# Optimization experiments

Measured on AMD Instinct MI355X. Metric: run time of the kernel, lower is better.

Reference implementation:

```python
import jax, jax.numpy as jnp
import numpy as np

EMBED_DIM = 1024
HEADS = 16
HEAD_DIM = EMBED_DIM // HEADS
N, SEQ = 2, 2048


def setup_inputs() -> dict:
    key = jax.random.key(0)
    ks = jax.random.split(key, 9)
    s = 1.0 / np.sqrt(HEAD_DIM)
    inp = {
        "values": jax.random.normal(ks[0], (N, SEQ, EMBED_DIM), jnp.float32),
        "keys": jax.random.normal(ks[1], (N, SEQ, EMBED_DIM), jnp.float32),
        "query": jax.random.normal(ks[2], (N, SEQ, EMBED_DIM), jnp.float32),
        "mask": jax.random.randint(ks[3], (N, 1, SEQ, SEQ), 0, 2, jnp.int32),
        # per-head projection weights (torch Linear: y = x @ W.T)
        "Wv": jax.random.normal(ks[4], (HEAD_DIM, HEAD_DIM), jnp.float32) * s,
        "Wk": jax.random.normal(ks[5], (HEAD_DIM, HEAD_DIM), jnp.float32) * s,
        "Wq": jax.random.normal(ks[6], (HEAD_DIM, HEAD_DIM), jnp.float32) * s,
        "Wo": jax.random.normal(ks[7], (EMBED_DIM, EMBED_DIM), jnp.float32) * (1.0 / np.sqrt(EMBED_DIM)),
        "bo": jax.random.normal(ks[8], (EMBED_DIM,), jnp.float32) * 0.01,
    }
    return inp


def reference(values, keys, query, mask, Wv, Wk, Wq, Wo, bo):
    n, q_len = query.shape[0], query.shape[1]
    v_len, k_len = values.shape[1], keys.shape[1]
    # reshape to [N, len, H, D]
    v = values.reshape(n, v_len, HEADS, HEAD_DIM)
    k = keys.reshape(n, k_len, HEADS, HEAD_DIM)
    q = query.reshape(n, q_len, HEADS, HEAD_DIM)
    # per-head linear projections (shared weight across heads), torch: x @ W.T
    v = jnp.einsum("nlhd,ed->nlhe", v, Wv)
    k = jnp.einsum("nlhd,ed->nlhe", k, Wk)
    q = jnp.einsum("nlhd,ed->nlhe", q, Wq)
    # energy: [N, H, Q, K]
    energy = jnp.einsum("nqhd,nkhd->nhqk", q, k)
    energy = jnp.where(mask == 0, jnp.float32(-1e20), energy)
    # NOTE: original scales by sqrt(embed_dim), not sqrt(head_dim)
    attention = jax.nn.softmax(energy / jnp.sqrt(jnp.float32(EMBED_DIM)), axis=3)
    out = jnp.einsum("nhql,nlhd->nqhd", attention, v).reshape(n, q_len, EMBED_DIM)
    out = out @ Wo.T + bo  # fc_out; dropout is identity in eval mode
    return out
```

## Files before the change

### kernel.cpp

```cpp
#include <hip/hip_runtime.h>
#include <hip/hip_bf16.h>

#define NB 2
#define SEQ 2048
#define HEADS 16
#define HD 64
#define ED 1024

typedef __bf16 bf16x8 __attribute__((ext_vector_type(8)));
typedef float f32x4 __attribute__((ext_vector_type(4)));
typedef unsigned short u16x8 __attribute__((ext_vector_type(8)));
typedef unsigned short u16x4 __attribute__((ext_vector_type(4)));

#if __has_builtin(__builtin_amdgcn_exp2f)
#define EXP2(x) __builtin_amdgcn_exp2f(x)
#else
#define EXP2(x) __builtin_exp2f(x)
#endif

__device__ __forceinline__ unsigned short f2bf(float f) {
    unsigned u = __builtin_bit_cast(unsigned, f);
    u += 0x7fffu + ((u >> 16) & 1u);
    return (unsigned short)(u >> 16);
}

__device__ __forceinline__ bf16x8 cvt8(const float* __restrict__ p) {
    const float4* p4 = (const float4*)p;
    float4 a = p4[0], b = p4[1];
    u16x8 u;
    u[0] = f2bf(a.x); u[1] = f2bf(a.y); u[2] = f2bf(a.z); u[3] = f2bf(a.w);
    u[4] = f2bf(b.x); u[5] = f2bf(b.y); u[6] = f2bf(b.z); u[7] = f2bf(b.w);
    return __builtin_bit_cast(bf16x8, u);
}

__device__ __forceinline__ bf16x8 ldfrag(const void* p) {
    uint4 v = *(const uint4*)p;
    return __builtin_bit_cast(bf16x8, v);
}

__device__ __forceinline__ f32x4 mfma16(bf16x8 a, bf16x8 b, f32x4 c) {
    return __builtin_amdgcn_mfma_f32_16x16x32_bf16(a, b, c, 0, 0, 0);
}

__device__ __forceinline__ unsigned packbf(float lo, float hi) {
    unsigned a = __builtin_bit_cast(unsigned, hi) + 0x8000u;
    unsigned b = __builtin_bit_cast(unsigned, lo) + 0x8000u;
    return __builtin_amdgcn_perm(a, b, 0x07060302u);
}

#define GLOAD_LDS(gp, lp) \
    __builtin_amdgcn_global_load_lds( \
        (const __attribute__((address_space(1))) unsigned int*)(gp), \
        (__attribute__((address_space(3))) unsigned int*)(lp), 16, 0, 0)

#define QSCALE 0.04508422f

__global__ __launch_bounds__(256) void proj_prep_kernel(
    const float* __restrict__ qin, const float* __restrict__ kin, const float* __restrict__ vin,
    const float* __restrict__ Wq, const float* __restrict__ Wk, const float* __restrict__ Wv,
    unsigned short* __restrict__ Qb, unsigned short* __restrict__ Kb,
    unsigned short* __restrict__ Vt,
    const int* __restrict__ mask, unsigned long long* __restrict__ bits,
    const float* __restrict__ Wo, unsigned short* __restrict__ Wob)
{
    __shared__ __align__(16) char tile[64 * 144];

    int bid = blockIdx.x;
    if (bid >= 3072) {
        int b2 = bid - 3072;
        if (b2 < NB * SEQ * SEQ / 256) {
            size_t i = (size_t)b2 * 256 + threadIdx.x;
            int m = mask[i];
            unsigned long long b = __ballot(m != 0);
            if ((threadIdx.x & 63) == 0) bits[i >> 6] = b;
        } else {
            size_t i = ((size_t)(b2 - NB * SEQ * SEQ / 256) * 256 + threadIdx.x) * 4;
            float4 v = *(const float4*)(Wo + i);
            u16x4 u;
            u[0] = f2bf(v.x); u[1] = f2bf(v.y); u[2] = f2bf(v.z); u[3] = f2bf(v.w);
            *(u16x4*)(Wob + i) = u;
        }
        return;
    }

    int t3  = bid >> 10;
    int rem = bid & 1023;
    int h   = rem >> 6;
    int rt  = rem & 63;
    int wave = threadIdx.x >> 6, lane = threadIdx.x & 63;
    int quad = lane >> 4, l16 = lane & 15;

    const float* in = (t3 == 0) ? qin : ((t3 == 1) ? kin : vin);
    const float* W  = (t3 == 0) ? Wq  : ((t3 == 1) ? Wk  : Wv);

    int r0 = rt * 64 + wave * 16;

    bf16x8 bf0[4], bf1[4];
#pragma unroll
    for (int sl = 0; sl < 4; ++sl) {
        const float* wrow = W + (sl * 16 + l16) * 64;
        bf0[sl] = cvt8(wrow + quad * 8);
        bf1[sl] = cvt8(wrow + 32 + quad * 8);
    }
    const float* xrow = in + (size_t)(r0 + l16) * ED + h * 64;
    bf16x8 af0 = cvt8(xrow + quad * 8);
    bf16x8 af1 = cvt8(xrow + 32 + quad * 8);

    f32x4 acc[4];
#pragma unroll
    for (int sl = 0; sl < 4; ++sl) {
        f32x4 c = {0.f, 0.f, 0.f, 0.f};
        c = mfma16(af0, bf0[sl], c);
        c = mfma16(af1, bf1[sl], c);
        acc[sl] = c;
    }
    float sc = (t3 == 0) ? QSCALE : 1.0f;

    size_t nh = (size_t)((r0 >> 11) * HEADS + h);
    int rl = lane >> 3, cl = lane & 7;

    if (t3 != 2) {
#pragma unroll
        for (int r = 0; r < 4; ++r) {
            int srow = wave * 16 + quad * 4 + r;
#pragma unroll
            for (int sl = 0; sl < 4; ++sl)
                *(unsigned short*)(tile + srow * 144 + (sl * 16 + l16) * 2) =
                    f2bf(acc[sl][r] * sc);
        }
        unsigned short* dst = (t3 == 0) ? Qb : Kb;
        int s0 = (r0 & 2047);
#pragma unroll
        for (int g = 0; g < 2; ++g) {
            int lrow = wave * 16 + g * 8 + rl;
            uint4 v = *(const uint4*)(tile + lrow * 144 + cl * 16);
            *(uint4*)(dst + (nh * SEQ + (s0 & ~15) + g * 8 + rl) * HD + cl * 8) = v;
        }
    } else {
#pragma unroll
        for (int r = 0; r < 4; ++r) {
            int srow = wave * 16 + quad * 4 + r;
#pragma unroll
            for (int sl = 0; sl < 4; ++sl)
                *(unsigned short*)(tile + (sl * 16 + l16) * 144 + srow * 2) =
                    f2bf(acc[sl][r]);
        }
        __syncthreads();
        int s_tile = rt & 31;
#pragma unroll
        for (int g = 0; g < 2; ++g) {
            int erow = wave * 16 + g * 8 + rl;
            uint4 v = *(const uint4*)(tile + erow * 144 + cl * 16);
            *(uint4*)(Vt + ((nh * 32 + s_tile) * 64 + erow) * 64 + cl * 8) = v;
        }
    }
}

__global__ __launch_bounds__(256, 4) void attn_kernel(
    const unsigned short* __restrict__ Qb, const unsigned short* __restrict__ Kb,
    const unsigned short* __restrict__ Vt2, const unsigned long long* __restrict__ mb,
    unsigned short* __restrict__ Ab)
{
    __shared__ __align__(16) char smem[24576 + 4 * 2304];

    int tid = threadIdx.x;
    int wave = tid >> 6, lane = tid & 63;
    int quad = lane >> 4, l16 = lane & 15;

    int b   = blockIdx.x;
    int xcd = b & 7;
    int j   = b >> 3;
    int nh  = xcd * 4 + (j >> 5);
    int qb  = j & 31;
    int n = nh >> 4, h = nh & 15;
    int q0 = qb * 64 + wave * 16;

    size_t headoff = (size_t)nh * SEQ * HD;
    const unsigned short* qrow = Qb + headoff + (size_t)(q0 + l16) * HD;
    bf16x8 qf0 = ldfrag(qrow + quad * 8);
    bf16x8 qf1 = ldfrag(qrow + 32 + quad * 8);

    int srow = lane >> 3, sslot = lane & 7;
    int stoff = srow * 128 + (((sslot - srow) & 7) * 16);

    int rotA = ((quad + l16) & 7) * 16;
    int aK0 = l16 * 128 + rotA;
    int aV  = 16384 + l16 * 128 + rotA;
    int aVx = aV ^ 64;
    char* pbase = smem + 24576 + wave * 2304;
    char* pw = pbase + l16 * 144 + quad * 8;
    char* pr = pbase + l16 * 144 + quad * 16;

    const unsigned short* gK = Kb + headoff;
    const unsigned short* gV = Vt2 + (size_t)nh * (32 * 4096);
    const unsigned long long* mbase = mb + (size_t)n * (SEQ * SEQ / 64)
                                         + (size_t)(q0 + l16) * (SEQ / 64);

    u16x8 ou;
#pragma unroll
    for (int jj = 0; jj < 8; ++jj) ou[jj] = 0x3F80;
    bf16x8 ones = __builtin_bit_cast(bf16x8, ou);

    f32x4 o[4] = {{0,0,0,0},{0,0,0,0},{0,0,0,0},{0,0,0,0}};
    f32x4 lacc = {0,0,0,0};
    int qsh = quad * 4;

    {
        const char* sK = (const char*)gK + stoff;
        const char* sV = (const char*)gV + stoff;
#pragma unroll
        for (int i2 = 0; i2 < 2; ++i2) {
            int c = wave * 2 + i2;
            GLOAD_LDS(sK + c * 1024, smem + c * 1024);
            GLOAD_LDS(sV + c * 1024, smem + 16384 + c * 1024);
        }
    }

    int par = 0;
    for (int kb = 0; kb < SEQ; kb += 64) {
        int kbn = (kb + 64) & (SEQ - 1);
        __syncthreads();
        {
            const char* sK = (const char*)(gK + (size_t)kbn * 64) + stoff;
            char* dK = smem + (par ^ 1) * 8192;
#pragma unroll
            for (int i2 = 0; i2 < 2; ++i2) {
                int c = wave * 2 + i2;
                GLOAD_LDS(sK + c * 1024, dK + c * 1024);
            }
        }
        unsigned long long m64 = mbase[kb >> 6] >> qsh;

        const char* kbuf = smem + par * 8192;
        bf16x8 kf[4][2];
#pragma unroll
        for (int kt = 0; kt < 4; ++kt) {
            kf[kt][0] = ldfrag(kbuf + aK0 + kt * 2048);
            kf[kt][1] = ldfrag(kbuf + (aK0 ^ 64) + kt * 2048);
        }
        f32x4 c[4];
#pragma unroll
        for (int kt = 0; kt < 4; ++kt) {
            f32x4 cc = {0.f, 0.f, 0.f, 0.f};
            cc = mfma16(kf[kt][0], qf0, cc);
            cc = mfma16(kf[kt][1], qf1, cc);
            c[kt] = cc;
        }
        unsigned mlo = (unsigned)m64;
        unsigned mhi = (unsigned)(m64 >> 32);
#pragma unroll
        for (int kt = 0; kt < 4; ++kt) {
            unsigned mw = (kt & 2) ? mhi : mlo;
            int bs = (kt & 1) ? 16 : 0;
            float p0 = ((mw >> (bs + 0)) & 1u) ? EXP2(c[kt][0]) : 0.f;
            float p1 = ((mw >> (bs + 1)) & 1u) ? EXP2(c[kt][1]) : 0.f;
            float p2 = ((mw >> (bs + 2)) & 1u) ? EXP2(c[kt][2]) : 0.f;
            float p3 = ((mw >> (bs + 3)) & 1u) ? EXP2(c[kt][3]) : 0.f;
            uint2 dw = { packbf(p0, p1), packbf(p2, p3) };
            *(uint2*)(pw + kt * 32) = dw;
        }
        bf16x8 pb0 = ldfrag(pr);
        bf16x8 pb1 = ldfrag(pr + 64);
        lacc = mfma16(ones, pb0, lacc);
        lacc = mfma16(ones, pb1, lacc);
#pragma unroll
        for (int sl = 0; sl < 4; ++sl) {
            o[sl] = mfma16(ldfrag(smem + aV  + sl * 2048), pb0, o[sl]);
            o[sl] = mfma16(ldfrag(smem + aVx + sl * 2048), pb1, o[sl]);
        }
        __syncthreads();
        {
            const char* sV = (const char*)(gV + (size_t)(kbn >> 6) * 4096) + stoff;
#pragma unroll
            for (int i2 = 0; i2 < 2; ++i2) {
                int c = wave * 2 + i2;
                GLOAD_LDS(sV + c * 1024, smem + 16384 + c * 1024);
            }
        }
        par ^= 1;
    }

    {
        float rinv = 1.0f / lacc[0];
        int q = q0 + l16;
        unsigned short* op = Ab + (((size_t)(n * SEQ + q)) * HEADS + h) * HD + qsh;
#pragma unroll
        for (int sl = 0; sl < 4; ++sl) {
            u16x4 u;
            u[0] = f2bf(o[sl][0] * rinv);
            u[1] = f2bf(o[sl][1] * rinv);
            u[2] = f2bf(o[sl][2] * rinv);
            u[3] = f2bf(o[sl][3] * rinv);
            *(u16x4*)(op + sl * 16) = u;
        }
    }
}

__global__ __launch_bounds__(256) void out_gemm_kernel(
    const unsigned short* __restrict__ Ab, const unsigned short* __restrict__ Wob,
    const float* __restrict__ bo, float* __restrict__ out)
{
    __shared__ __align__(16) char lds[49152];

    int tid = threadIdx.x;
    int wave = tid >> 6, lane = tid & 63;
    int quad = lane >> 4, l16 = lane & 15;
    int rt = blockIdx.x >> 4, ct = blockIdx.x & 15;
    int wr = wave >> 1, wc = wave & 1;

    int srow = lane >> 3, sslot = lane & 7;
    int stoff = srow * 2048 + (((sslot - srow) & 7) * 16);
    const char* gA = (const char*)Ab  + (size_t)rt * 128 * 2048 + stoff;
    const char* gB = (const char*)Wob + (size_t)ct * 64 * 2048 + stoff;

    int aA[4], aB[2];
#pragma unroll
    for (int i = 0; i < 4; ++i) {
        int rowA = wr * 64 + i * 16 + l16;
        aA[i] = rowA * 128 + (((quad + rowA) & 7) * 16);
    }
#pragma unroll
    for (int sl = 0; sl < 2; ++sl) {
        int rowB = wc * 32 + sl * 16 + l16;
        aB[sl] = rowB * 128 + (((quad + rowB) & 7) * 16);
    }

#pragma unroll
    for (int i = 0; i < 4; ++i) {
        int c = wave * 4 + i;
        GLOAD_LDS(gA + (size_t)c * 16384, lds + c * 1024);
    }
#pragma unroll
    for (int i = 0; i < 2; ++i) {
        int c = wave * 2 + i;
        GLOAD_LDS(gB + (size_t)c * 16384, lds + 32768 + c * 1024);
    }

    f32x4 acc[4][2] = {};
    int par = 0;
    for (int f = 0; f < ED; f += 64) {
        int fn = (f + 64) & (ED - 1);
        __syncthreads();
        {
            int pA = (par ^ 1) * 16384;
            int pB = 32768 + (par ^ 1) * 8192;
#pragma unroll
            for (int i = 0; i < 4; ++i) {
                int c = wave * 4 + i;
                GLOAD_LDS(gA + (size_t)c * 16384 + fn * 2, lds + pA + c * 1024);
            }
#pragma unroll
            for (int i = 0; i < 2; ++i) {
                int c = wave * 2 + i;
                GLOAD_LDS(gB + (size_t)c * 16384 + fn * 2, lds + pB + c * 1024);
            }
        }
        int bA = par * 16384;
        int bB = 32768 + par * 8192;
#pragma unroll
        for (int kk = 0; kk < 2; ++kk) {
            int x = kk * 64;
            bf16x8 af[4], bfr[2];
#pragma unroll
            for (int i = 0; i < 4; ++i)    af[i]  = ldfrag(lds + bA + (aA[i] ^ x));
#pragma unroll
            for (int sl = 0; sl < 2; ++sl) bfr[sl] = ldfrag(lds + bB + (aB[sl] ^ x));
#pragma unroll
            for (int i = 0; i < 4; ++i)
#pragma unroll
                for (int sl = 0; sl < 2; ++sl)
                    acc[i][sl] = mfma16(af[i], bfr[sl], acc[i][sl]);
        }
        par ^= 1;
    }

    float bv[2];
#pragma unroll
    for (int sl = 0; sl < 2; ++sl)
        bv[sl] = bo[ct * 64 + wc * 32 + sl * 16 + l16];
#pragma unroll
    for (int i = 0; i < 4; ++i)
#pragma unroll
        for (int r = 0; r < 4; ++r) {
            int row = rt * 128 + wr * 64 + i * 16 + quad * 4 + r;
#pragma unroll
            for (int sl = 0; sl < 2; ++sl) {
                int e = ct * 64 + wc * 32 + sl * 16 + l16;
                out[(size_t)row * ED + e] = acc[i][sl][r] + bv[sl];
            }
        }
}

extern "C" void kernel_launch(void* const* d_in, const int* in_sizes, int n_in,
                              void* d_out, int out_size, void* d_ws, size_t ws_size,
                              hipStream_t stream)
{
    const float* values = (const float*)d_in[0];
    const float* keys   = (const float*)d_in[1];
    const float* query  = (const float*)d_in[2];
    const int*   mask   = (const int*)d_in[3];
    const float* Wv     = (const float*)d_in[4];
    const float* Wk     = (const float*)d_in[5];
    const float* Wq     = (const float*)d_in[6];
    const float* Wo     = (const float*)d_in[7];
    const float* bo     = (const float*)d_in[8];
    float* out = (float*)d_out;

    char* w = (char*)d_ws;
    unsigned short* Qb  = (unsigned short*)(w);
    unsigned short* Kb  = (unsigned short*)(w +  8388608);
    unsigned short* Vt  = (unsigned short*)(w + 16777216);
    unsigned short* Ab  = (unsigned short*)(w + 25165824);
    unsigned long long* Mb = (unsigned long long*)(w + 33554432);
    unsigned short* Wob = (unsigned short*)(w + 34603008);

    proj_prep_kernel<<<3072 + NB * SEQ * SEQ / 256 + ED * ED / 1024, 256, 0, stream>>>(
        query, keys, values, Wq, Wk, Wv, Qb, Kb, Vt, mask, Mb, Wo, Wob);
    attn_kernel<<<1024, 256, 0, stream>>>(Qb, Kb, Vt, Mb, Ab);
    out_gemm_kernel<<<512, 256, 0, stream>>>(Ab, Wob, bo, out);
}
```

Before: 231.4 us.

## Double-buffer V tiles, prefetch mask word, and swizzle P scratch layout

V tiles move from a single LDS buffer into a double buffer, so both the next K and the next V tile are prefetched at the top of each iteration. This removes the second __syncthreads per loop iteration and the serialized V load that followed the PV MFMAs. The mask word for the next block is loaded one iteration ahead, and the P scratch moves from a padded 144-byte row stride to a 128-byte XOR-swizzled layout to avoid bank conflicts. LDS use grows from about 33KB to 40KB per block, which could reduce occupancy at 4 blocks per CU.

```diff
diff --git a/kernel.cpp b/kernel.cpp
--- a/kernel.cpp
+++ b/kernel.cpp
@@ -161,7 +161,7 @@
     const unsigned short* __restrict__ Vt2, const unsigned long long* __restrict__ mb,
     unsigned short* __restrict__ Ab)
 {
-    __shared__ __align__(16) char smem[24576 + 4 * 2304];
+    __shared__ __align__(16) char smem[32768 + 4 * 2048];
 
     int tid = threadIdx.x;
     int wave = tid >> 6, lane = tid & 63;
@@ -184,12 +184,12 @@
     int stoff = srow * 128 + (((sslot - srow) & 7) * 16);
 
     int rotA = ((quad + l16) & 7) * 16;
-    int aK0 = l16 * 128 + rotA;
-    int aV  = 16384 + l16 * 128 + rotA;
-    int aVx = aV ^ 64;
-    char* pbase = smem + 24576 + wave * 2304;
-    char* pw = pbase + l16 * 144 + quad * 8;
-    char* pr = pbase + l16 * 144 + quad * 16;
+    int aKV = l16 * 128 + rotA;
+
+    int pswz = (l16 & 3) << 5;
+    char* prow = smem + 32768 + wave * 2048 + l16 * 128;
+    char* pw  = prow + quad * 8;
+    int  proff = (quad * 16) ^ pswz;
 
     const unsigned short* gK = Kb + headoff;
     const unsigned short* gV = Vt2 + (size_t)nh * (32 * 4096);
@@ -215,6 +215,7 @@
             GLOAD_LDS(sV + c * 1024, smem + 16384 + c * 1024);
         }
     }
+    unsigned long long mnext = mbase[0] >> qsh;
 
     int par = 0;
     for (int kb = 0; kb < SEQ; kb += 64) {
@@ -222,21 +223,25 @@
         __syncthreads();
         {
             const char* sK = (const char*)(gK + (size_t)kbn * 64) + stoff;
+            const char* sV = (const char*)(gV + (size_t)(kbn >> 6) * 4096) + stoff;
             char* dK = smem + (par ^ 1) * 8192;
+            char* dV = smem + 16384 + (par ^ 1) * 8192;
 #pragma unroll
             for (int i2 = 0; i2 < 2; ++i2) {
                 int c = wave * 2 + i2;
                 GLOAD_LDS(sK + c * 1024, dK + c * 1024);
+                GLOAD_LDS(sV + c * 1024, dV + c * 1024);
             }
         }
-        unsigned long long m64 = mbase[kb >> 6] >> qsh;
+        unsigned long long m64 = mnext;
+        mnext = mbase[kbn >> 6] >> qsh;
 
         const char* kbuf = smem + par * 8192;
         bf16x8 kf[4][2];
 #pragma unroll
         for (int kt = 0; kt < 4; ++kt) {
-            kf[kt][0] = ldfrag(kbuf + aK0 + kt * 2048);
-            kf[kt][1] = ldfrag(kbuf + (aK0 ^ 64) + kt * 2048);
+            kf[kt][0] = ldfrag(kbuf + aKV + kt * 2048);
+            kf[kt][1] = ldfrag(kbuf + (aKV ^ 64) + kt * 2048);
         }
         f32x4 c[4];
 #pragma unroll
@@ -257,25 +262,17 @@
             float p2 = ((mw >> (bs + 2)) & 1u) ? EXP2(c[kt][2]) : 0.f;
             float p3 = ((mw >> (bs + 3)) & 1u) ? EXP2(c[kt][3]) : 0.f;
             uint2 dw = { packbf(p0, p1), packbf(p2, p3) };
-            *(uint2*)(pw + kt * 32) = dw;
-        }
-        bf16x8 pb0 = ldfrag(pr);
-        bf16x8 pb1 = ldfrag(pr + 64);
+            *(uint2*)(pw + ((kt * 32) ^ pswz)) = dw;
+        }
+        bf16x8 pb0 = ldfrag(prow + proff);
+        bf16x8 pb1 = ldfrag(prow + (proff ^ 64));
         lacc = mfma16(ones, pb0, lacc);
         lacc = mfma16(ones, pb1, lacc);
+        const char* vbuf = smem + 16384 + par * 8192;
 #pragma unroll
         for (int sl = 0; sl < 4; ++sl) {
-            o[sl] = mfma16(ldfrag(smem + aV  + sl * 2048), pb0, o[sl]);
-            o[sl] = mfma16(ldfrag(smem + aVx + sl * 2048), pb1, o[sl]);
-        }
-        __syncthreads();
-        {
-            const char* sV = (const char*)(gV + (size_t)(kbn >> 6) * 4096) + stoff;
-#pragma unroll
-            for (int i2 = 0; i2 < 2; ++i2) {
-                int c = wave * 2 + i2;
-                GLOAD_LDS(sV + c * 1024, smem + 16384 + c * 1024);
-            }
+            o[sl] = mfma16(ldfrag(vbuf + aKV + sl * 2048), pb0, o[sl]);
+            o[sl] = mfma16(ldfrag(vbuf + (aKV ^ 64) + sl * 2048), pb1, o[sl]);
         }
         par ^= 1;
     }
```

After: 238.7 us. +3.1%, slower.
